# Performance work log

Measured on AMD Instinct MI355X. Metric: run time of the kernel, lower is better.

## Reference

```python
import jax, jax.numpy as jnp
import numpy as np

B, T, I, H = 64, 1024, 512, 512


def setup_inputs() -> dict:
    key = jax.random.key(0)
    ks = jax.random.split(key, 5)
    s = 1.0 / np.sqrt(H)  # PyTorch nn.RNN init scale
    X = jax.random.normal(ks[0], (B, T, I), dtype=jnp.float32)
    W_ih = jax.random.uniform(ks[1], (H, I), minval=-s, maxval=s, dtype=jnp.float32)
    W_hh = jax.random.uniform(ks[2], (H, H), minval=-s, maxval=s, dtype=jnp.float32)
    b_ih = jax.random.uniform(ks[3], (H,), minval=-s, maxval=s, dtype=jnp.float32)
    b_hh = jax.random.uniform(ks[4], (H,), minval=-s, maxval=s, dtype=jnp.float32)
    return {"X": X, "W_ih": W_ih, "W_hh": W_hh, "b_ih": b_ih, "b_hh": b_hh}


def reference(X, W_ih, W_hh, b_ih, b_hh):
    # h_t = tanh(W_ih x_t + b_ih + W_hh h_{t-1} + b_hh)  (PyTorch nn.RNN, tanh)
    # Batch the input-to-hidden GEMM over all timesteps up front.
    Xp = jnp.einsum('bti,hi->bth', X, W_ih) + b_ih + b_hh  # [B,T,H]
    Wt = W_hh.T

    def step(h, xt):
        h = jnp.tanh(xt + h @ Wt)
        return h, h

    h0 = jnp.zeros((X.shape[0], W_hh.shape[0]), dtype=X.dtype)
    _, ys = jax.lax.scan(step, h0, jnp.swapaxes(Xp, 0, 1))  # scan over T
    return jnp.swapaxes(ys, 0, 1)  # [B,T,H]
```

## Files before the change

kernel.cpp:

```cpp
#include <hip/hip_runtime.h>
#include <hip/hip_fp16.h>

typedef unsigned int u32;
typedef _Float16 h2v __attribute__((ext_vector_type(2)));

#define B_ 64
#define T_ 1024
#define H_ 512
#define I_ 512

__device__ __forceinline__ float dot2f(u32 w, u32 h, float acc) {
#if __has_builtin(__builtin_amdgcn_fdot2)
    return __builtin_amdgcn_fdot2(__builtin_bit_cast(h2v, w),
                                  __builtin_bit_cast(h2v, h), acc, false);
#else
    __half2 a = __builtin_bit_cast(__half2, w);
    __half2 b = __builtin_bit_cast(__half2, h);
    return acc + __low2float(a) * __low2float(b) + __high2float(a) * __high2float(b);
#endif
}

__device__ __forceinline__ u32 pkf16(float a, float b) {
    __half2 h = __floats2half2_rn(a, b);
    return __builtin_bit_cast(u32, h);
}

template <int CTRL>
__device__ __forceinline__ float prs_dpp(float a, float b, bool bit) {
    float keep = bit ? b : a;
    float give = bit ? a : b;
    int gv = __builtin_bit_cast(int, give);
    float got = __builtin_bit_cast(float,
        __builtin_amdgcn_update_dpp(0, gv, CTRL, 0xF, 0xF, true));
    return keep + got;
}
__device__ __forceinline__ float prs_shfl4(float a, float b, bool bit) {
    float keep = bit ? b : a;
    float give = bit ? a : b;
    return keep + __shfl_xor(give, 4);
}

__global__ void prep_w(const float* __restrict__ Whh, u32* __restrict__ wreg,
                       u32* __restrict__ wlds) {
    const int tid = threadIdx.x;
    const int g = tid >> 3, sub = tid & 7;
    const int bid = blockIdx.x;
    if (bid < 224) {
        const int r = bid, o = r >> 5, k5 = r & 31;
        const int j = g * 8 + o, i = sub * 64 + 2 * k5;
        wreg[r * 512 + tid] = pkf16(Whh[j * H_ + i], Whh[j * H_ + i + 1]);
    } else {
        const int c = bid - 224;
        const int j = g * 8 + 7;
        for (int q = 0; q < 4; q++) {
            const int k5 = c * 4 + q;
            const int i = sub * 64 + 2 * k5;
            wlds[c * 2048 + tid * 4 + q] = pkf16(Whh[j * H_ + i], Whh[j * H_ + i + 1]);
        }
    }
}

#define BM 128
#define BN 64

__launch_bounds__(256, 3)
__global__ void gemm_xp(const float* __restrict__ X, const float* __restrict__ Wih,
                        const float* __restrict__ bih, const float* __restrict__ bhh,
                        float* __restrict__ out) {
    __shared__ u32 Xs[16][BM + 4];
    __shared__ u32 Ws[16][BN + 4];
    const int t = threadIdx.x;
    const int bn = blockIdx.x & 7;
    const int bm = blockIdx.x >> 3;
    const int m0 = bm * BM, n0 = bn * BN;
    const int tm = t & 15, tn = t >> 4;
    float acc[8][4];
#pragma unroll
    for (int i = 0; i < 8; i++)
#pragma unroll
        for (int j = 0; j < 4; j++) acc[i][j] = 0.f;
    const int kc = t & 7, rr = t >> 3;
    const int key = ((tm >> 2) & 1) << 2;
    for (int kt = 0; kt < 16; kt++) {
        const int k0 = kt * 32;
#pragma unroll
        for (int it = 0; it < 4; it++) {
            const int m = it * 32 + rr;
            float4 v = *(const float4*)&X[(size_t)(m0 + m) * I_ + k0 + kc * 4];
            const int mp = m ^ (((m >> 5) & 1) << 2);
            Xs[kc * 2 + 0][mp] = pkf16(v.x, v.y);
            Xs[kc * 2 + 1][mp] = pkf16(v.z, v.w);
        }
#pragma unroll
        for (int it = 0; it < 2; it++) {
            const int n = it * 32 + rr;
            float4 v = *(const float4*)&Wih[(size_t)(n0 + n) * I_ + k0 + kc * 4];
            Ws[kc * 2 + 0][n] = pkf16(v.x, v.y);
            Ws[kc * 2 + 1][n] = pkf16(v.z, v.w);
        }
        __syncthreads();
#pragma unroll
        for (int k2 = 0; k2 < 16; k2++) {
            uint4 a0 = *(const uint4*)&Xs[k2][(tm * 8) ^ key];
            uint4 a1 = *(const uint4*)&Xs[k2][(tm * 8 + 4) ^ key];
            uint4 bv = *(const uint4*)&Ws[k2][tn * 4];
            u32 aa[8] = {a0.x, a0.y, a0.z, a0.w, a1.x, a1.y, a1.z, a1.w};
            u32 bb[4] = {bv.x, bv.y, bv.z, bv.w};
#pragma unroll
            for (int mi = 0; mi < 8; mi++)
#pragma unroll
                for (int ni = 0; ni < 4; ni++)
                    acc[mi][ni] = dot2f(aa[mi], bb[ni], acc[mi][ni]);
        }
        __syncthreads();
    }
    float4 b1 = *(const float4*)&bih[n0 + tn * 4];
    float4 b2 = *(const float4*)&bhh[n0 + tn * 4];
    float4 bs = {b1.x + b2.x, b1.y + b2.y, b1.z + b2.z, b1.w + b2.w};
#pragma unroll
    for (int mi = 0; mi < 8; mi++) {
        const int row = m0 + tm * 8 + mi;
        float4 st = {acc[mi][0] + bs.x, acc[mi][1] + bs.y,
                     acc[mi][2] + bs.z, acc[mi][3] + bs.w};
        *(float4*)&out[(size_t)row * H_ + n0 + tn * 4] = st;
    }
}


#define STEP_K(k, hval)                                         \
    acc0 = dot2f(w2[0 * 32 + cc * 8 + k], (hval), acc0);        \
    acc1 = dot2f(w2[1 * 32 + cc * 8 + k], (hval), acc1);        \
    acc2 = dot2f(w2[2 * 32 + cc * 8 + k], (hval), acc2);        \
    acc3 = dot2f(w2[3 * 32 + cc * 8 + k], (hval), acc3);        \
    acc4 = dot2f(w2[4 * 32 + cc * 8 + k], (hval), acc4);        \
    acc5 = dot2f(w2[5 * 32 + cc * 8 + k], (hval), acc5);        \
    acc6 = dot2f(w2[6 * 32 + cc * 8 + k], (hval), acc6);

__launch_bounds__(512)
__attribute__((amdgpu_waves_per_eu(2, 2)))
__global__ void rnn_scan(const u32* __restrict__ wreg, const u32* __restrict__ wlds_g,
                         float* __restrict__ out) {
    __shared__ u32 wl[16384];
    __shared__ u32 hh[512];
    const int tid = threadIdx.x;
    const int sub = tid & 7;
    u32 w2[224];
#pragma unroll
    for (int r = 0; r < 224; r++) w2[r] = wreg[r * 512 + tid];
#pragma unroll
    for (int i = 0; i < 32; i++) wl[i * 512 + tid] = wlds_g[i * 512 + tid];
    hh[tid] = 0u;
    __syncthreads();
    float* p = out + (size_t)blockIdx.x * (T_ * H_) + tid;
    const int xorkey = sub << 2;
    __half* hhh = reinterpret_cast<__half*>(hh);
    const int wv = tid >> 1;
    const int wslot = (wv ^ (((wv >> 5) & 7) << 2)) * 2 + (tid & 1);
    const int wbase = tid << 2;
    const bool b0 = (sub & 1) != 0, b1 = (sub & 2) != 0, b2 = (sub & 4) != 0;
    for (int t = 0; t < T_; t++) {
        const float xp = *p;
        const int rb = (t & 1) << 8;
        float acc0 = 0.f, acc1 = 0.f, acc2 = 0.f, acc3 = 0.f;
        float acc4 = 0.f, acc5 = 0.f, acc6 = 0.f, acc7 = 0.f;
#pragma unroll
        for (int cc = 0; cc < 4; cc++) {
            uint4 hA = *(const uint4*)&hh[rb + ((sub * 32 + cc * 8) ^ xorkey)];
            uint4 w7a = *(const uint4*)&wl[(cc * 2) * 2048 + wbase];
            STEP_K(0, hA.x); acc7 = dot2f(w7a.x, hA.x, acc7);
            STEP_K(1, hA.y); acc7 = dot2f(w7a.y, hA.y, acc7);
            STEP_K(2, hA.z); acc7 = dot2f(w7a.z, hA.z, acc7);
            STEP_K(3, hA.w); acc7 = dot2f(w7a.w, hA.w, acc7);
            uint4 hB = *(const uint4*)&hh[rb + ((sub * 32 + cc * 8 + 4) ^ xorkey)];
            uint4 w7b = *(const uint4*)&wl[(cc * 2 + 1) * 2048 + wbase];
            STEP_K(4, hB.x); acc7 = dot2f(w7b.x, hB.x, acc7);
            STEP_K(5, hB.y); acc7 = dot2f(w7b.y, hB.y, acc7);
            STEP_K(6, hB.z); acc7 = dot2f(w7b.z, hB.z, acc7);
            STEP_K(7, hB.w); acc7 = dot2f(w7b.w, hB.w, acc7);
        }
        float s0 = prs_dpp<0xB1>(acc0, acc1, b0);
        float s2 = prs_dpp<0xB1>(acc2, acc3, b0);
        float s4 = prs_dpp<0xB1>(acc4, acc5, b0);
        float s6 = prs_dpp<0xB1>(acc6, acc7, b0);
        float u0 = prs_dpp<0x4E>(s0, s2, b1);
        float u4 = prs_dpp<0x4E>(s4, s6, b1);
        float r  = prs_shfl4(u0, u4, b2);
        const float pre = xp + r;
        const float e = __expf(-2.f * fabsf(pre));
        const float th = __builtin_copysignf((1.f - e) / (1.f + e), pre);
        *p = th;
        p += H_;
        hhh[(((t & 1) ^ 1) << 9) + wslot] = __float2half(th);
        asm volatile("s_waitcnt lgkmcnt(0)" ::: "memory");
        __builtin_amdgcn_sched_barrier(0);
        __builtin_amdgcn_s_barrier();
        __builtin_amdgcn_sched_barrier(0);
    }
}

extern "C" void kernel_launch(void* const* d_in, const int* in_sizes, int n_in,
                              void* d_out, int out_size, void* d_ws, size_t ws_size,
                              hipStream_t stream) {
    const float* X    = (const float*)d_in[0];
    const float* Wih  = (const float*)d_in[1];
    const float* Whh  = (const float*)d_in[2];
    const float* bih  = (const float*)d_in[3];
    const float* bhh  = (const float*)d_in[4];
    float* out = (float*)d_out;
    u32* wreg = (u32*)d_ws;
    u32* wlds = wreg + 114688;

    prep_w<<<dim3(232), dim3(512), 0, stream>>>(Whh, wreg, wlds);
    gemm_xp<<<dim3((65536 / BM) * (H_ / BN)), dim3(256), 0, stream>>>(X, Wih, bih, bhh, out);
    rnn_scan<<<dim3(B_), dim3(512), 0, stream>>>(wreg, wlds, out);
}
```

Measured before the change: 1.986 ms.

## Move half of row-6 weights to LDS and prefetch LDS weights across timesteps

The recurrent weights are repartitioned so that output row 6 for the last two k-chunks moves from registers into LDS. This frees 16 VGPRs per thread. The freed registers hold the LDS-resident weights for rows 6 and 7, and those weights are now loaded at the end of each timestep for the next one. The goal is to take LDS weight-load latency off the critical path of the serial scan, at the cost of more LDS use and a more complex weight layout in prep_w.

New measurement: 4.009 ms. +101.8%, slower.

```diff
diff --git a/kernel.cpp b/kernel.cpp
--- a/kernel.cpp
+++ b/kernel.cpp
@@ -45,15 +45,19 @@
     const int tid = threadIdx.x;
     const int g = tid >> 3, sub = tid & 7;
     const int bid = blockIdx.x;
-    if (bid < 224) {
-        const int r = bid, o = r >> 5, k5 = r & 31;
+    if (bid < 208) {
+        const int r = bid;
+        const int o  = (r < 192) ? (r >> 5) : 6;
+        const int k5 = (r < 192) ? (r & 31) : (r - 192);
         const int j = g * 8 + o, i = sub * 64 + 2 * k5;
         wreg[r * 512 + tid] = pkf16(Whh[j * H_ + i], Whh[j * H_ + i + 1]);
     } else {
-        const int c = bid - 224;
-        const int j = g * 8 + 7;
+        const int c = bid - 208;
+        int j, cc, half;
+        if (c < 4) { cc = 2 + (c >> 1); half = c & 1; j = g * 8 + 6; }
+        else       { int c7 = c - 4; cc = c7 >> 1; half = c7 & 1; j = g * 8 + 7; }
         for (int q = 0; q < 4; q++) {
-            const int k5 = c * 4 + q;
+            const int k5 = cc * 8 + half * 4 + q;
             const int i = sub * 64 + 2 * k5;
             wlds[c * 2048 + tid * 4 + q] = pkf16(Whh[j * H_ + i], Whh[j * H_ + i + 1]);
         }
@@ -127,28 +131,42 @@
 }
 
 
-#define STEP_K(k, hval)                                         \
-    acc0 = dot2f(w2[0 * 32 + cc * 8 + k], (hval), acc0);        \
-    acc1 = dot2f(w2[1 * 32 + cc * 8 + k], (hval), acc1);        \
-    acc2 = dot2f(w2[2 * 32 + cc * 8 + k], (hval), acc2);        \
-    acc3 = dot2f(w2[3 * 32 + cc * 8 + k], (hval), acc3);        \
-    acc4 = dot2f(w2[4 * 32 + cc * 8 + k], (hval), acc4);        \
-    acc5 = dot2f(w2[5 * 32 + cc * 8 + k], (hval), acc5);        \
-    acc6 = dot2f(w2[6 * 32 + cc * 8 + k], (hval), acc6);
+#define CCBLOCK(CO, W6EXPR_A, W6EXPR_B, P7A, P7B)                               \
+    {                                                                           \
+        uint4 hA = *(const uint4*)&hh[rb + ((sub * 32 + (CO)*8) ^ xorkey)];     \
+        uint4 hB = *(const uint4*)&hh[rb + ((sub * 32 + (CO)*8 + 4) ^ xorkey)]; \
+        u32 h8[8]  = {hA.x, hA.y, hA.z, hA.w, hB.x, hB.y, hB.z, hB.w};          \
+        u32 w6c[8] = {W6EXPR_A.x, W6EXPR_A.y, W6EXPR_A.z, W6EXPR_A.w,           \
+                      W6EXPR_B.x, W6EXPR_B.y, W6EXPR_B.z, W6EXPR_B.w};          \
+        u32 w7c[8] = {P7A.x, P7A.y, P7A.z, P7A.w, P7B.x, P7B.y, P7B.z, P7B.w};  \
+        _Pragma("unroll")                                                       \
+        for (int k = 0; k < 8; k++) {                                           \
+            acc0 = dot2f(w2[  0 + (CO)*8 + k], h8[k], acc0);                    \
+            acc1 = dot2f(w2[ 32 + (CO)*8 + k], h8[k], acc1);                    \
+            acc2 = dot2f(w2[ 64 + (CO)*8 + k], h8[k], acc2);                    \
+            acc3 = dot2f(w2[ 96 + (CO)*8 + k], h8[k], acc3);                    \
+            acc4 = dot2f(w2[128 + (CO)*8 + k], h8[k], acc4);                    \
+            acc5 = dot2f(w2[160 + (CO)*8 + k], h8[k], acc5);                    \
+            acc6 = dot2f(w6c[k], h8[k], acc6);                                  \
+            acc7 = dot2f(w7c[k], h8[k], acc7);                                  \
+        }                                                                       \
+    }
+
+struct u4x { u32 x, y, z, w; };
 
 __launch_bounds__(512)
 __attribute__((amdgpu_waves_per_eu(2, 2)))
 __global__ void rnn_scan(const u32* __restrict__ wreg, const u32* __restrict__ wlds_g,
                          float* __restrict__ out) {
-    __shared__ u32 wl[16384];
+    __shared__ u32 wl[24576];
     __shared__ u32 hh[512];
     const int tid = threadIdx.x;
     const int sub = tid & 7;
-    u32 w2[224];
-#pragma unroll
-    for (int r = 0; r < 224; r++) w2[r] = wreg[r * 512 + tid];
-#pragma unroll
-    for (int i = 0; i < 32; i++) wl[i * 512 + tid] = wlds_g[i * 512 + tid];
+    u32 w2[208];
+#pragma unroll
+    for (int r = 0; r < 208; r++) w2[r] = wreg[r * 512 + tid];
+#pragma unroll
+    for (int i = 0; i < 48; i++) wl[i * 512 + tid] = wlds_g[i * 512 + tid];
     hh[tid] = 0u;
     __syncthreads();
     float* p = out + (size_t)blockIdx.x * (T_ * H_) + tid;
@@ -157,34 +175,47 @@
     const int wv = tid >> 1;
     const int wslot = (wv ^ (((wv >> 5) & 7) << 2)) * 2 + (tid & 1);
     const int wbase = tid << 2;
-    const bool b0 = (sub & 1) != 0, b1 = (sub & 2) != 0, b2 = (sub & 4) != 0;
+    const bool bb0 = (sub & 1) != 0, bb1 = (sub & 2) != 0, bb2 = (sub & 4) != 0;
+
+    uint4 p6a2, p6b2, p6a3, p6b3;
+    uint4 p7a0, p7b0, p7a1, p7b1, p7a2, p7b2, p7a3, p7b3;
+#define PREFETCH_W()                                                \
+    p6a2 = *(const uint4*)&wl[0 * 2048 + wbase];                    \
+    p6b2 = *(const uint4*)&wl[1 * 2048 + wbase];                    \
+    p6a3 = *(const uint4*)&wl[2 * 2048 + wbase];                    \
+    p6b3 = *(const uint4*)&wl[3 * 2048 + wbase];                    \
+    p7a0 = *(const uint4*)&wl[8192 + 0 * 2048 + wbase];             \
+    p7b0 = *(const uint4*)&wl[8192 + 1 * 2048 + wbase];             \
+    p7a1 = *(const uint4*)&wl[8192 + 2 * 2048 + wbase];             \
+    p7b1 = *(const uint4*)&wl[8192 + 3 * 2048 + wbase];             \
+    p7a2 = *(const uint4*)&wl[8192 + 4 * 2048 + wbase];             \
+    p7b2 = *(const uint4*)&wl[8192 + 5 * 2048 + wbase];             \
+    p7a3 = *(const uint4*)&wl[8192 + 6 * 2048 + wbase];             \
+    p7b3 = *(const uint4*)&wl[8192 + 7 * 2048 + wbase];
+
+    PREFETCH_W();
+
     for (int t = 0; t < T_; t++) {
         const float xp = *p;
         const int rb = (t & 1) << 8;
         float acc0 = 0.f, acc1 = 0.f, acc2 = 0.f, acc3 = 0.f;
         float acc4 = 0.f, acc5 = 0.f, acc6 = 0.f, acc7 = 0.f;
-#pragma unroll
-        for (int cc = 0; cc < 4; cc++) {
-            uint4 hA = *(const uint4*)&hh[rb + ((sub * 32 + cc * 8) ^ xorkey)];
-            uint4 w7a = *(const uint4*)&wl[(cc * 2) * 2048 + wbase];
-            STEP_K(0, hA.x); acc7 = dot2f(w7a.x, hA.x, acc7);
-            STEP_K(1, hA.y); acc7 = dot2f(w7a.y, hA.y, acc7);
-            STEP_K(2, hA.z); acc7 = dot2f(w7a.z, hA.z, acc7);
-            STEP_K(3, hA.w); acc7 = dot2f(w7a.w, hA.w, acc7);
-            uint4 hB = *(const uint4*)&hh[rb + ((sub * 32 + cc * 8 + 4) ^ xorkey)];
-            uint4 w7b = *(const uint4*)&wl[(cc * 2 + 1) * 2048 + wbase];
-            STEP_K(4, hB.x); acc7 = dot2f(w7b.x, hB.x, acc7);
-            STEP_K(5, hB.y); acc7 = dot2f(w7b.y, hB.y, acc7);
-            STEP_K(6, hB.z); acc7 = dot2f(w7b.z, hB.z, acc7);
-            STEP_K(7, hB.w); acc7 = dot2f(w7b.w, hB.w, acc7);
-        }
-        float s0 = prs_dpp<0xB1>(acc0, acc1, b0);
-        float s2 = prs_dpp<0xB1>(acc2, acc3, b0);
-        float s4 = prs_dpp<0xB1>(acc4, acc5, b0);
-        float s6 = prs_dpp<0xB1>(acc6, acc7, b0);
-        float u0 = prs_dpp<0x4E>(s0, s2, b1);
-        float u4 = prs_dpp<0x4E>(s4, s6, b1);
-        float r  = prs_shfl4(u0, u4, b2);
+        u4x q60 = {w2[192], w2[193], w2[194], w2[195]};
+        u4x q61 = {w2[196], w2[197], w2[198], w2[199]};
+        u4x q62 = {w2[200], w2[201], w2[202], w2[203]};
+        u4x q63 = {w2[204], w2[205], w2[206], w2[207]};
+        CCBLOCK(0, q60, q61, p7a0, p7b0)
+        CCBLOCK(1, q62, q63, p7a1, p7b1)
+        CCBLOCK(2, p6a2, p6b2, p7a2, p7b2)
+        CCBLOCK(3, p6a3, p6b3, p7a3, p7b3)
+        PREFETCH_W();
+        float s0 = prs_dpp<0xB1>(acc0, acc1, bb0);
+        float s2 = prs_dpp<0xB1>(acc2, acc3, bb0);
+        float s4 = prs_dpp<0xB1>(acc4, acc5, bb0);
+        float s6 = prs_dpp<0xB1>(acc6, acc7, bb0);
+        float u0 = prs_dpp<0x4E>(s0, s2, bb1);
+        float u4 = prs_dpp<0x4E>(s4, s6, bb1);
+        float r  = prs_shfl4(u0, u4, bb2);
         const float pre = xp + r;
         const float e = __expf(-2.f * fabsf(pre));
         const float th = __builtin_copysignf((1.f - e) / (1.f + e), pre);
@@ -208,9 +239,9 @@
     const float* bhh  = (const float*)d_in[4];
     float* out = (float*)d_out;
     u32* wreg = (u32*)d_ws;
-    u32* wlds = wreg + 114688;
-
-    prep_w<<<dim3(232), dim3(512), 0, stream>>>(Whh, wreg, wlds);
+    u32* wlds = wreg + 106496;
+
+    prep_w<<<dim3(220), dim3(512), 0, stream>>>(Whh, wreg, wlds);
     gemm_xp<<<dim3((65536 / BM) * (H_ / BN)), dim3(256), 0, stream>>>(X, Wih, bih, bhh, out);
     rnn_scan<<<dim3(B_), dim3(512), 0, stream>>>(wreg, wlds, out);
 }
```

## Split RNN recurrence across two blocks per batch row with global flag sync

Applied to the files above, without the earlier changes.

Each batch row's hidden-state matvec is now split over two workgroups, each holding half of W_hh (transposed, fp16) in registers and computing a partial dot product per output. The partials are exchanged through a global buffer with per-block release/acquire flags and a spin-wait every timestep. The weight prep kernel is simplified to a transposed packing. This halves per-thread math and register pressure but adds a global-memory round trip and an inter-block handshake on the serial critical path of every step.

Measured after the change: 4.897 ms. +146.5%, slower.

```diff
diff --git a/kernel.cpp b/kernel.cpp
--- a/kernel.cpp
+++ b/kernel.cpp
@@ -25,39 +25,10 @@
     return __builtin_bit_cast(u32, h);
 }
 
-template <int CTRL>
-__device__ __forceinline__ float prs_dpp(float a, float b, bool bit) {
-    float keep = bit ? b : a;
-    float give = bit ? a : b;
-    int gv = __builtin_bit_cast(int, give);
-    float got = __builtin_bit_cast(float,
-        __builtin_amdgcn_update_dpp(0, gv, CTRL, 0xF, 0xF, true));
-    return keep + got;
-}
-__device__ __forceinline__ float prs_shfl4(float a, float b, bool bit) {
-    float keep = bit ? b : a;
-    float give = bit ? a : b;
-    return keep + __shfl_xor(give, 4);
-}
-
-__global__ void prep_w(const float* __restrict__ Whh, u32* __restrict__ wreg,
-                       u32* __restrict__ wlds) {
-    const int tid = threadIdx.x;
-    const int g = tid >> 3, sub = tid & 7;
-    const int bid = blockIdx.x;
-    if (bid < 224) {
-        const int r = bid, o = r >> 5, k5 = r & 31;
-        const int j = g * 8 + o, i = sub * 64 + 2 * k5;
-        wreg[r * 512 + tid] = pkf16(Whh[j * H_ + i], Whh[j * H_ + i + 1]);
-    } else {
-        const int c = bid - 224;
-        const int j = g * 8 + 7;
-        for (int q = 0; q < 4; q++) {
-            const int k5 = c * 4 + q;
-            const int i = sub * 64 + 2 * k5;
-            wlds[c * 2048 + tid * 4 + q] = pkf16(Whh[j * H_ + i], Whh[j * H_ + i + 1]);
-        }
-    }
+__global__ void prep_wT(const float* __restrict__ Whh, u32* __restrict__ wT) {
+    const int k2 = blockIdx.x;
+    const int o = threadIdx.x;
+    wT[k2 * 512 + o] = pkf16(Whh[o * 512 + 2 * k2], Whh[o * 512 + 2 * k2 + 1]);
 }
 
 #define BM 128
@@ -126,75 +97,60 @@
     }
 }
 
+__launch_bounds__(512)
+__global__ void rnn_scan(const u32* __restrict__ wT, float* __restrict__ out,
+                         float* __restrict__ pbuf, u32* __restrict__ flags) {
+    __shared__ __align__(16) u32 hh[2][256];
+    const int tid = threadIdx.x;
+    const int blk = blockIdx.x;
+    const int b = blk >> 1, kh = blk & 1;
+    const int o = tid;
 
-#define STEP_K(k, hval)                                         \
-    acc0 = dot2f(w2[0 * 32 + cc * 8 + k], (hval), acc0);        \
-    acc1 = dot2f(w2[1 * 32 + cc * 8 + k], (hval), acc1);        \
-    acc2 = dot2f(w2[2 * 32 + cc * 8 + k], (hval), acc2);        \
-    acc3 = dot2f(w2[3 * 32 + cc * 8 + k], (hval), acc3);        \
-    acc4 = dot2f(w2[4 * 32 + cc * 8 + k], (hval), acc4);        \
-    acc5 = dot2f(w2[5 * 32 + cc * 8 + k], (hval), acc5);        \
-    acc6 = dot2f(w2[6 * 32 + cc * 8 + k], (hval), acc6);
+    u32 wr[128];
+#pragma unroll
+    for (int r = 0; r < 128; r++) wr[r] = wT[(kh * 128 + r) * 512 + o];
 
-__launch_bounds__(512)
-__attribute__((amdgpu_waves_per_eu(2, 2)))
-__global__ void rnn_scan(const u32* __restrict__ wreg, const u32* __restrict__ wlds_g,
-                         float* __restrict__ out) {
-    __shared__ u32 wl[16384];
-    __shared__ u32 hh[512];
-    const int tid = threadIdx.x;
-    const int sub = tid & 7;
-    u32 w2[224];
+    ((u32*)hh)[tid] = 0u;
+    __syncthreads();
+
+    float* outb = out + (size_t)b * (T_ * H_);
+    float xp = outb[o];
+
+    for (int t = 0; t < T_; t++) {
+        const int buf = t & 1;
+        float acc = 0.f;
 #pragma unroll
-    for (int r = 0; r < 224; r++) w2[r] = wreg[r * 512 + tid];
-#pragma unroll
-    for (int i = 0; i < 32; i++) wl[i * 512 + tid] = wlds_g[i * 512 + tid];
-    hh[tid] = 0u;
-    __syncthreads();
-    float* p = out + (size_t)blockIdx.x * (T_ * H_) + tid;
-    const int xorkey = sub << 2;
-    __half* hhh = reinterpret_cast<__half*>(hh);
-    const int wv = tid >> 1;
-    const int wslot = (wv ^ (((wv >> 5) & 7) << 2)) * 2 + (tid & 1);
-    const int wbase = tid << 2;
-    const bool b0 = (sub & 1) != 0, b1 = (sub & 2) != 0, b2 = (sub & 4) != 0;
-    for (int t = 0; t < T_; t++) {
-        const float xp = *p;
-        const int rb = (t & 1) << 8;
-        float acc0 = 0.f, acc1 = 0.f, acc2 = 0.f, acc3 = 0.f;
-        float acc4 = 0.f, acc5 = 0.f, acc6 = 0.f, acc7 = 0.f;
-#pragma unroll
-        for (int cc = 0; cc < 4; cc++) {
-            uint4 hA = *(const uint4*)&hh[rb + ((sub * 32 + cc * 8) ^ xorkey)];
-            uint4 w7a = *(const uint4*)&wl[(cc * 2) * 2048 + wbase];
-            STEP_K(0, hA.x); acc7 = dot2f(w7a.x, hA.x, acc7);
-            STEP_K(1, hA.y); acc7 = dot2f(w7a.y, hA.y, acc7);
-            STEP_K(2, hA.z); acc7 = dot2f(w7a.z, hA.z, acc7);
-            STEP_K(3, hA.w); acc7 = dot2f(w7a.w, hA.w, acc7);
-            uint4 hB = *(const uint4*)&hh[rb + ((sub * 32 + cc * 8 + 4) ^ xorkey)];
-            uint4 w7b = *(const uint4*)&wl[(cc * 2 + 1) * 2048 + wbase];
-            STEP_K(4, hB.x); acc7 = dot2f(w7b.x, hB.x, acc7);
-            STEP_K(5, hB.y); acc7 = dot2f(w7b.y, hB.y, acc7);
-            STEP_K(6, hB.z); acc7 = dot2f(w7b.z, hB.z, acc7);
-            STEP_K(7, hB.w); acc7 = dot2f(w7b.w, hB.w, acc7);
+        for (int i = 0; i < 32; i++) {
+            uint4 hq = *(const uint4*)&hh[buf][kh * 128 + i * 4];
+            acc = dot2f(wr[i * 4 + 0], hq.x, acc);
+            acc = dot2f(wr[i * 4 + 1], hq.y, acc);
+            acc = dot2f(wr[i * 4 + 2], hq.z, acc);
+            acc = dot2f(wr[i * 4 + 3], hq.w, acc);
         }
-        float s0 = prs_dpp<0xB1>(acc0, acc1, b0);
-        float s2 = prs_dpp<0xB1>(acc2, acc3, b0);
-        float s4 = prs_dpp<0xB1>(acc4, acc5, b0);
-        float s6 = prs_dpp<0xB1>(acc6, acc7, b0);
-        float u0 = prs_dpp<0x4E>(s0, s2, b1);
-        float u4 = prs_dpp<0x4E>(s4, s6, b1);
-        float r  = prs_shfl4(u0, u4, b2);
-        const float pre = xp + r;
+        float* pb_w = pbuf + ((size_t)buf * 128 + blk) * 512;
+        float* pb_p = pbuf + ((size_t)buf * 128 + (blk ^ 1)) * 512;
+        __hip_atomic_store(pb_w + o, acc, __ATOMIC_RELAXED, __HIP_MEMORY_SCOPE_AGENT);
+        asm volatile("s_waitcnt vmcnt(0)" ::: "memory");
+        __syncthreads();
+        if (tid == 0) {
+            __hip_atomic_store(&flags[blk], (u32)(t + 1), __ATOMIC_RELEASE,
+                               __HIP_MEMORY_SCOPE_AGENT);
+            while (__hip_atomic_load(&flags[blk ^ 1], __ATOMIC_ACQUIRE,
+                                     __HIP_MEMORY_SCOPE_AGENT) < (u32)(t + 1)) {
+                __builtin_amdgcn_s_sleep(1);
+            }
+        }
+        __syncthreads();
+        const float theirs = __hip_atomic_load(pb_p + o, __ATOMIC_RELAXED,
+                                               __HIP_MEMORY_SCOPE_AGENT);
+        const float s = kh ? (theirs + acc) : (acc + theirs);
+        const float pre = xp + s;
         const float e = __expf(-2.f * fabsf(pre));
         const float th = __builtin_copysignf((1.f - e) / (1.f + e), pre);
-        *p = th;
-        p += H_;
-        hhh[(((t & 1) ^ 1) << 9) + wslot] = __float2half(th);
-        asm volatile("s_waitcnt lgkmcnt(0)" ::: "memory");
-        __builtin_amdgcn_sched_barrier(0);
-        __builtin_amdgcn_s_barrier();
-        __builtin_amdgcn_sched_barrier(0);
+        if (!kh) outb[(size_t)t * H_ + o] = th;
+        xp = (t + 1 < T_) ? outb[(size_t)(t + 1) * H_ + o] : 0.f;
+        ((__half*)hh)[((buf ^ 1) << 9) + o] = __float2half(th);
+        __syncthreads();
     }
 }
 
@@ -207,10 +163,13 @@
     const float* bih  = (const float*)d_in[3];
     const float* bhh  = (const float*)d_in[4];
     float* out = (float*)d_out;
-    u32* wreg = (u32*)d_ws;
-    u32* wlds = wreg + 114688;
 
-    prep_w<<<dim3(232), dim3(512), 0, stream>>>(Whh, wreg, wlds);
+    u32*   wT    = (u32*)d_ws;
+    float* pbuf  = (float*)((char*)d_ws + 524288);
+    u32*   flags = (u32*)((char*)d_ws + 1048576);
+
+    hipMemsetAsync(flags, 0, 128 * sizeof(u32), stream);
+    prep_wT<<<dim3(256), dim3(512), 0, stream>>>(Whh, wT);
     gemm_xp<<<dim3((65536 / BM) * (H_ / BN)), dim3(256), 0, stream>>>(X, Wih, bih, bhh, out);
-    rnn_scan<<<dim3(B_), dim3(512), 0, stream>>>(wreg, wlds, out);
+    rnn_scan<<<dim3(2 * B_), dim3(512), 0, stream>>>(wT, out, pbuf, flags);
 }
```
